# Kernel optimization log

Hardware: AMD Instinct MI355X
Metric: run time of the kernel (lower is better)

## Reference

```python
import jax, jax.numpy as jnp
import numpy as np

B, C, T, H = 256, 8, 512, 512  # batch, channels(6 arms + 2 time), timesteps, hidden
OUT = 2


def setup_inputs() -> dict:
    key = jax.random.key(0)
    ks = jax.random.split(key, 8)
    # arm lengths positive and away from 0 (denominator 0.15*arm in likelihood)
    arms = jax.random.uniform(ks[0], (B, 6, T), minval=0.5, maxval=1.5)
    tm = jax.random.uniform(ks[1], (B, 2, T))
    inputs = jnp.concatenate([arms, tm], axis=1)  # (B, 8, T)
    s_in = 1.0 / np.sqrt(6.0)
    s_rec = 1.0 / np.sqrt(float(H))
    W_in = jax.random.uniform(ks[2], (H, 6), minval=-s_in, maxval=s_in)
    b_in = jax.random.uniform(ks[3], (H,), minval=-s_in, maxval=s_in)
    W_rec = jax.random.uniform(ks[4], (H, H), minval=-s_rec, maxval=s_rec)
    b_rec = jax.random.uniform(ks[5], (H,), minval=-s_rec, maxval=s_rec)
    W_key = jax.random.uniform(ks[6], (OUT, H), minval=-s_rec, maxval=s_rec)
    b_key = jax.random.uniform(ks[7], (OUT,), minval=-s_rec, maxval=s_rec)
    return {"inputs": inputs, "W_in": W_in, "b_in": b_in,
            "W_rec": W_rec, "b_rec": b_rec, "W_key": W_key, "b_key": b_key}


def _likelihood(tm, arms):
    # tm: (B,), arms: (B, n) -> squared normalized timing mismatch; zero rows where tm==0
    prs = jnp.square((tm[:, None] - arms) / (0.15 * arms))
    return jnp.where(tm[:, None] == 0, 0.0, prs)


def reference(inputs, W_in, b_in, W_rec, b_rec, W_key, b_key):
    Bn, Cn, Tn = inputs.shape
    Hn = W_rec.shape[0]
    xs = jnp.transpose(inputs, (2, 0, 1))[1:]  # (T-1, B, 8); loop starts at t=1
    key0 = jnp.ones((Bn,), dtype=inputs.dtype)
    h0 = jnp.zeros((Bn, Hn), dtype=inputs.dtype)

    def step(carry, x_t):
        key_h_pre, h_pre = carry
        arms_pri = x_t[:, :2]
        arms_sec = x_t[:, 2:6]
        tm = x_t[:, 6:8]
        # gate secondary arms by previous key
        arms_sum = arms_sec[:, :2] * key_h_pre[:, None] + arms_sec[:, 2:] * (1.0 - key_h_pre)[:, None]
        prs_t = jnp.concatenate([_likelihood(tm[:, 0], arms_pri),
                                 _likelihood(tm[:, 1], arms_sum)], axis=1)  # (B, 4)
        inp_t = jnp.concatenate([arms_pri, arms_sum, tm], axis=1)  # (B, 6)
        h_t = jnp.tanh(inp_t @ W_in.T + b_in + h_pre @ W_rec.T + b_rec)  # (B, H)
        key_t = jax.nn.sigmoid(h_t @ W_key.T + b_key)  # (B, 2)
        return (key_t[:, 0], h_t), (key_t, prs_t, h_t)

    _, (keys, prs, hs) = jax.lax.scan(step, (key0, h0), xs)
    # prepend the t=0 zero slice and move time to last axis, matching torch buffers
    keys = jnp.concatenate([jnp.zeros((1, Bn, OUT), keys.dtype), keys], axis=0).transpose(1, 2, 0)
    prs = jnp.concatenate([jnp.zeros((1, Bn, 2 * OUT), prs.dtype), prs], axis=0).transpose(1, 2, 0)
    hs = jnp.concatenate([jnp.zeros((1, Bn, Hn), hs.dtype), hs], axis=0).transpose(1, 2, 0)
    tm_modified = inputs[:, -2:, :]
    return keys, prs, hs, tm_modified
```

## Files before the change

kernel.cpp:

```cpp
#include <hip/hip_runtime.h>

#define TDS 512
#define NBATCH 256

typedef _Float16 h2 __attribute__((ext_vector_type(2)));

__device__ __forceinline__ unsigned int pack2(float lo, float hi) {
    h2 v;
    v.x = (_Float16)lo;
    v.y = (_Float16)hi;
    return __builtin_bit_cast(unsigned int, v);
}
__device__ __forceinline__ h2 uph(unsigned int u) {
    return __builtin_bit_cast(h2, u);
}

#if __has_builtin(__builtin_amdgcn_fdot2)
__device__ __forceinline__ float fdot2(h2 w, h2 x, float acc) {
    return __builtin_amdgcn_fdot2(w, x, acc, false);
}
#else
__device__ __forceinline__ float fdot2(h2 w, h2 x, float acc) {
    return fmaf((float)w.x, (float)x.x, fmaf((float)w.y, (float)x.y, acc));
}
#endif

__device__ __forceinline__ float fast_rcp(float x) {
#if __has_builtin(__builtin_amdgcn_rcpf)
    return __builtin_amdgcn_rcpf(x);
#else
    return 1.0f / x;
#endif
}

__device__ __forceinline__ float fast_tanh(float x) {
    return 1.0f - 2.0f * fast_rcp(1.0f + __expf(2.0f * x));
}
__device__ __forceinline__ float fast_sigmoid(float x) {
    return fast_rcp(1.0f + __expf(-x));
}

#define KEYS_OFF 0u
#define PRS_OFF  262144u
#define HS_OFF   786432u
#define TM_OFF   67895296u

#define HP_CHUNK 72
#define HP_BUF   (4 * HP_CHUNK)

__device__ __forceinline__ void flush_window(
    float* __restrict__ g_out, int b, int tid, int w,
    const float* __restrict__ lds_hst,
    const float (*__restrict__ lds_kst)[2],
    const float (*__restrict__ lds_pst)[4])
{
    const int tbase = w * 8;
    float h[8];
#pragma unroll
    for (int s = 0; s < 8; ++s) h[s] = lds_hst[s * TDS + tid];
    float4* dst = (float4*)(g_out + HS_OFF + (unsigned)b * 262144u + (unsigned)tid * 512u + (unsigned)tbase);
    dst[0] = make_float4(h[0], h[1], h[2], h[3]);
    dst[1] = make_float4(h[4], h[5], h[6], h[7]);

    if (tid < 2) {
        float k[8];
#pragma unroll
        for (int s = 0; s < 8; ++s) k[s] = lds_kst[s][tid];
        float4* kd = (float4*)(g_out + KEYS_OFF + (unsigned)b * 1024u + (unsigned)tid * 512u + (unsigned)tbase);
        kd[0] = make_float4(k[0], k[1], k[2], k[3]);
        kd[1] = make_float4(k[4], k[5], k[6], k[7]);
    } else if (tid < 6) {
        const int o = tid - 2;
        float p[8];
#pragma unroll
        for (int s = 0; s < 8; ++s) p[s] = lds_pst[s][o];
        float4* pd = (float4*)(g_out + PRS_OFF + (unsigned)b * 2048u + (unsigned)o * 512u + (unsigned)tbase);
        pd[0] = make_float4(p[0], p[1], p[2], p[3]);
        pd[1] = make_float4(p[4], p[5], p[6], p[7]);
    }
}

__global__ __launch_bounds__(TDS, 1) void rnn_att_kernel(
    const float* __restrict__ g_inputs,
    const float* __restrict__ g_Win,
    const float* __restrict__ g_bin,
    const float* __restrict__ g_Wrec,
    const float* __restrict__ g_brec,
    const float* __restrict__ g_Wkey,
    const float* __restrict__ g_bkey,
    float* __restrict__ g_out)
{
    __shared__ __attribute__((aligned(16))) unsigned int lds_w[64][TDS];
    __shared__ __attribute__((aligned(16))) unsigned int lds_hp[2 * HP_BUF];
    __shared__ __attribute__((aligned(16))) float lds_hst[8 * TDS];
    __shared__ __attribute__((aligned(16))) float lds_ksum[2][16];
    __shared__ float lds_kst[8][2];
    __shared__ float lds_pst[8][4];

    const int tid = threadIdx.x;
    const int b = blockIdx.x;
    const int kc = tid & 3;
    const int rg = tid >> 2;
    const int r_out = tid;

    unsigned int wreg[192];
#pragma unroll
    for (int i = 0; i < 4; ++i) {
        const int r = (rg << 2) + i;
        const float4* src = (const float4*)(g_Wrec + r * 512 + kc * 128);
#pragma unroll
        for (int g = 0; g < 16; ++g) {
            float4 f0 = src[2 * g];
            float4 f1 = src[2 * g + 1];
            unsigned int u0 = pack2(f0.x, f0.y);
            unsigned int u1 = pack2(f0.z, f0.w);
            unsigned int u2 = pack2(f1.x, f1.y);
            unsigned int u3 = pack2(f1.z, f1.w);
            if (g < 12) {
                wreg[i * 48 + g * 4 + 0] = u0;
                wreg[i * 48 + g * 4 + 1] = u1;
                wreg[i * 48 + g * 4 + 2] = u2;
                wreg[i * 48 + g * 4 + 3] = u3;
            } else {
                const int pbase = i * 16 + (g - 12) * 4;
                lds_w[pbase + 0][tid] = u0;
                lds_w[pbase + 1][tid] = u1;
                lds_w[pbase + 2][tid] = u2;
                lds_w[pbase + 3][tid] = u3;
            }
        }
    }

    float win[6];
#pragma unroll
    for (int j = 0; j < 6; ++j) win[j] = g_Win[r_out * 6 + j];
    const float bias = g_bin[r_out] + g_brec[r_out];
    const float wk0 = g_Wkey[r_out];
    const float wk1 = g_Wkey[512 + r_out];
    const float bk0 = g_bkey[0];
    const float bk1 = g_bkey[1];

    lds_hp[tid] = 0u;
    if (tid < 2 * HP_BUF - TDS) lds_hp[TDS + tid] = 0u;

    if (tid < 256) {
        const float4* s = (const float4*)(g_inputs + b * 4096 + 3072);
        float4* d = (float4*)(g_out + TM_OFF + (unsigned)b * 1024u);
        d[tid] = s[tid];
    }
    __syncthreads();

    const float* gin = g_inputs + b * 4096;
    float key_pre = 1.0f;
    float xv[8];

    for (int t = 0; t < 512; ++t) {
        const int s = t & 7;
        if (s == 0 && t > 0) {
            __syncthreads();
            flush_window(g_out, b, tid, (t >> 3) - 1, lds_hst, lds_kst, lds_pst);
            __syncthreads();
        }

        float xn[8];
        {
            const int tn = (t < 511) ? t + 1 : 511;
#pragma unroll
            for (int j = 0; j < 8; ++j) xn[j] = gin[512 * j + tn];
        }

        float h_new = 0.0f, p0 = 0.0f, p1 = 0.0f, p2 = 0.0f, p3 = 0.0f;
        if (t > 0) {
            float x0 = xv[0], x1 = xv[1], x2 = xv[2], x3 = xv[3];
            float x4 = xv[4], x5 = xv[5], x6 = xv[6], x7 = xv[7];
            float as0 = x2 * key_pre + x4 * (1.0f - key_pre);
            float as1 = x3 * key_pre + x5 * (1.0f - key_pre);
            float wd = bias;
            wd = fmaf(x0, win[0], wd);
            wd = fmaf(x1, win[1], wd);
            wd = fmaf(as0, win[2], wd);
            wd = fmaf(as1, win[3], wd);
            wd = fmaf(x6, win[4], wd);
            wd = fmaf(x7, win[5], wd);
            {
                float q0 = (x6 - x0) / (0.15f * x0);
                float q1 = (x6 - x1) / (0.15f * x1);
                float q2 = (x7 - as0) / (0.15f * as0);
                float q3 = (x7 - as1) / (0.15f * as1);
                p0 = q0 * q0; p1 = q1 * q1; p2 = q2 * q2; p3 = q3 * q3;
                if (x6 == 0.0f) { p0 = 0.0f; p1 = 0.0f; }
                if (x7 == 0.0f) { p2 = 0.0f; p3 = 0.0f; }
            }
            const unsigned int* hb = lds_hp + ((t - 1) & 1) * HP_BUF + kc * HP_CHUNK;
            float a[4] = {0.0f, 0.0f, 0.0f, 0.0f};
#pragma unroll
            for (int c = 0; c < 12; ++c) {
                uint4 hu = ((const uint4*)hb)[c];
                h2 x0h = uph(hu.x), x1h = uph(hu.y), x2h = uph(hu.z), x3h = uph(hu.w);
#pragma unroll
                for (int i = 0; i < 4; ++i) {
                    a[i] = fdot2(uph(wreg[i * 48 + 4 * c + 0]), x0h, a[i]);
                    a[i] = fdot2(uph(wreg[i * 48 + 4 * c + 1]), x1h, a[i]);
                    a[i] = fdot2(uph(wreg[i * 48 + 4 * c + 2]), x2h, a[i]);
                    a[i] = fdot2(uph(wreg[i * 48 + 4 * c + 3]), x3h, a[i]);
                }
            }
#pragma unroll
            for (int c = 0; c < 4; ++c) {
                uint4 hu = ((const uint4*)(hb + 48))[c];
                h2 x0h = uph(hu.x), x1h = uph(hu.y), x2h = uph(hu.z), x3h = uph(hu.w);
#pragma unroll
                for (int i = 0; i < 4; ++i) {
                    a[i] = fdot2(uph(lds_w[i * 16 + 4 * c + 0][tid]), x0h, a[i]);
                    a[i] = fdot2(uph(lds_w[i * 16 + 4 * c + 1][tid]), x1h, a[i]);
                    a[i] = fdot2(uph(lds_w[i * 16 + 4 * c + 2][tid]), x2h, a[i]);
                    a[i] = fdot2(uph(lds_w[i * 16 + 4 * c + 3][tid]), x3h, a[i]);
                }
            }
#pragma unroll
            for (int i = 0; i < 4; ++i) {
                a[i] += __shfl_xor(a[i], 1, 64);
                a[i] += __shfl_xor(a[i], 2, 64);
            }
            float rsum = a[0];
            if (kc == 1) rsum = a[1];
            if (kc == 2) rsum = a[2];
            if (kc == 3) rsum = a[3];
            h_new = fast_tanh(rsum + wd);

            float h_other = __shfl_xor(h_new, 1, 64);
            if ((tid & 1) == 0) {
                const int p = tid >> 1;
                lds_hp[(t & 1) * HP_BUF + (p >> 6) * HP_CHUNK + (p & 63)] = pack2(h_new, h_other);
            }

            float kp0 = h_new * wk0, kp1 = h_new * wk1;
#pragma unroll
            for (int m = 1; m < 64; m <<= 1) {
                kp0 += __shfl_xor(kp0, m, 64);
                kp1 += __shfl_xor(kp1, m, 64);
            }
            if ((tid & 63) == 0) {
                lds_ksum[t & 1][(tid >> 6) * 2 + 0] = kp0;
                lds_ksum[t & 1][(tid >> 6) * 2 + 1] = kp1;
            }
            if (tid == 0) {
                lds_pst[s][0] = p0; lds_pst[s][1] = p1;
                lds_pst[s][2] = p2; lds_pst[s][3] = p3;
            }
        } else {
            if (tid == 0) {
                lds_pst[s][0] = 0.0f; lds_pst[s][1] = 0.0f;
                lds_pst[s][2] = 0.0f; lds_pst[s][3] = 0.0f;
            }
        }
        lds_hst[s * TDS + r_out] = h_new;

        __syncthreads();

        float k0 = 0.0f, k1 = 0.0f;
        if (t > 0) {
            const float4* ks = (const float4*)&lds_ksum[t & 1][0];
            float4 v0 = ks[0], v1 = ks[1], v2 = ks[2], v3 = ks[3];
            float s0 = ((v0.x + v1.x) + (v2.x + v3.x)) + ((v0.z + v1.z) + (v2.z + v3.z));
            float s1 = ((v0.y + v1.y) + (v2.y + v3.y)) + ((v0.w + v1.w) + (v2.w + v3.w));
            k0 = fast_sigmoid(s0 + bk0);
            k1 = fast_sigmoid(s1 + bk1);
            key_pre = k0;
        }
        if (tid == 0) { lds_kst[s][0] = k0; lds_kst[s][1] = k1; }

#pragma unroll
        for (int j = 0; j < 8; ++j) xv[j] = xn[j];
    }

    __syncthreads();
    flush_window(g_out, b, tid, 63, lds_hst, lds_kst, lds_pst);
}

extern "C" void kernel_launch(void* const* d_in, const int* in_sizes, int n_in,
                              void* d_out, int out_size, void* d_ws, size_t ws_size,
                              hipStream_t stream) {
    rnn_att_kernel<<<dim3(NBATCH), dim3(TDS), 0, stream>>>(
        (const float*)d_in[0],
        (const float*)d_in[1],
        (const float*)d_in[2],
        (const float*)d_in[3],
        (const float*)d_in[4],
        (const float*)d_in[5],
        (const float*)d_in[6],
        (float*)d_out);
}
```

Before: 1.898 ms.

## Restructure RNN time loop to one barrier per step with double-buffered staging

Rotates the loop so the key reduction from the previous step is read right after the single per-step barrier. The separate flush barriers are removed by double-buffering the key and likelihood staging arrays and passing the current key in registers. The key-dependent input projection is refactored into a single fma, and the likelihood divisions move to thread 0 using fast reciprocals. This cuts the barriers per step from one plus two every eight steps down to one, at the cost of slightly lower likelihood precision and more intricate slot and parity indexing.

Measured after the change: 2.016 ms. 1.06x slower.

```diff
diff --git a/kernel.cpp b/kernel.cpp
--- a/kernel.cpp
+++ b/kernel.cpp
@@ -51,8 +51,9 @@
 __device__ __forceinline__ void flush_window(
     float* __restrict__ g_out, int b, int tid, int w,
     const float* __restrict__ lds_hst,
-    const float (*__restrict__ lds_kst)[2],
-    const float (*__restrict__ lds_pst)[4])
+    const float (*__restrict__ kst)[2],
+    const float (*__restrict__ pst)[4],
+    float k0loc, float k1loc)
 {
     const int tbase = w * 8;
     float h[8];
@@ -65,7 +66,8 @@
     if (tid < 2) {
         float k[8];
 #pragma unroll
-        for (int s = 0; s < 8; ++s) k[s] = lds_kst[s][tid];
+        for (int s = 0; s < 7; ++s) k[s] = kst[s][tid];
+        k[7] = (tid == 0) ? k0loc : k1loc;
         float4* kd = (float4*)(g_out + KEYS_OFF + (unsigned)b * 1024u + (unsigned)tid * 512u + (unsigned)tbase);
         kd[0] = make_float4(k[0], k[1], k[2], k[3]);
         kd[1] = make_float4(k[4], k[5], k[6], k[7]);
@@ -73,7 +75,7 @@
         const int o = tid - 2;
         float p[8];
 #pragma unroll
-        for (int s = 0; s < 8; ++s) p[s] = lds_pst[s][o];
+        for (int s = 0; s < 8; ++s) p[s] = pst[s][o];
         float4* pd = (float4*)(g_out + PRS_OFF + (unsigned)b * 2048u + (unsigned)o * 512u + (unsigned)tbase);
         pd[0] = make_float4(p[0], p[1], p[2], p[3]);
         pd[1] = make_float4(p[4], p[5], p[6], p[7]);
@@ -94,8 +96,8 @@
     __shared__ __attribute__((aligned(16))) unsigned int lds_hp[2 * HP_BUF];
     __shared__ __attribute__((aligned(16))) float lds_hst[8 * TDS];
     __shared__ __attribute__((aligned(16))) float lds_ksum[2][16];
-    __shared__ float lds_kst[8][2];
-    __shared__ float lds_pst[8][4];
+    __shared__ float lds_kst[2][8][2];
+    __shared__ float lds_pst[2][8][4];
 
     const int tid = threadIdx.x;
     const int b = blockIdx.x;
@@ -148,134 +150,152 @@
         float4* d = (float4*)(g_out + TM_OFF + (unsigned)b * 1024u);
         d[tid] = s[tid];
     }
+
+    lds_hst[tid] = 0.0f;
+    if (tid == 0) {
+        lds_pst[0][0][0] = 0.0f; lds_pst[0][0][1] = 0.0f;
+        lds_pst[0][0][2] = 0.0f; lds_pst[0][0][3] = 0.0f;
+        lds_kst[0][0][0] = 0.0f; lds_kst[0][0][1] = 0.0f;
+    }
     __syncthreads();
 
     const float* gin = g_inputs + b * 4096;
     float key_pre = 1.0f;
     float xv[8];
-
-    for (int t = 0; t < 512; ++t) {
-        const int s = t & 7;
-        if (s == 0 && t > 0) {
-            __syncthreads();
-            flush_window(g_out, b, tid, (t >> 3) - 1, lds_hst, lds_kst, lds_pst);
-            __syncthreads();
-        }
-
-        float xn[8];
-        {
-            const int tn = (t < 511) ? t + 1 : 511;
-#pragma unroll
-            for (int j = 0; j < 8; ++j) xn[j] = gin[512 * j + tn];
-        }
-
-        float h_new = 0.0f, p0 = 0.0f, p1 = 0.0f, p2 = 0.0f, p3 = 0.0f;
-        if (t > 0) {
-            float x0 = xv[0], x1 = xv[1], x2 = xv[2], x3 = xv[3];
-            float x4 = xv[4], x5 = xv[5], x6 = xv[6], x7 = xv[7];
-            float as0 = x2 * key_pre + x4 * (1.0f - key_pre);
-            float as1 = x3 * key_pre + x5 * (1.0f - key_pre);
-            float wd = bias;
-            wd = fmaf(x0, win[0], wd);
-            wd = fmaf(x1, win[1], wd);
-            wd = fmaf(as0, win[2], wd);
-            wd = fmaf(as1, win[3], wd);
-            wd = fmaf(x6, win[4], wd);
-            wd = fmaf(x7, win[5], wd);
-            {
-                float q0 = (x6 - x0) / (0.15f * x0);
-                float q1 = (x6 - x1) / (0.15f * x1);
-                float q2 = (x7 - as0) / (0.15f * as0);
-                float q3 = (x7 - as1) / (0.15f * as1);
-                p0 = q0 * q0; p1 = q1 * q1; p2 = q2 * q2; p3 = q3 * q3;
-                if (x6 == 0.0f) { p0 = 0.0f; p1 = 0.0f; }
-                if (x7 == 0.0f) { p2 = 0.0f; p3 = 0.0f; }
-            }
-            const unsigned int* hb = lds_hp + ((t - 1) & 1) * HP_BUF + kc * HP_CHUNK;
-            float a[4] = {0.0f, 0.0f, 0.0f, 0.0f};
-#pragma unroll
-            for (int c = 0; c < 12; ++c) {
-                uint4 hu = ((const uint4*)hb)[c];
-                h2 x0h = uph(hu.x), x1h = uph(hu.y), x2h = uph(hu.z), x3h = uph(hu.w);
-#pragma unroll
-                for (int i = 0; i < 4; ++i) {
-                    a[i] = fdot2(uph(wreg[i * 48 + 4 * c + 0]), x0h, a[i]);
-                    a[i] = fdot2(uph(wreg[i * 48 + 4 * c + 1]), x1h, a[i]);
-                    a[i] = fdot2(uph(wreg[i * 48 + 4 * c + 2]), x2h, a[i]);
-                    a[i] = fdot2(uph(wreg[i * 48 + 4 * c + 3]), x3h, a[i]);
-                }
-            }
-#pragma unroll
-            for (int c = 0; c < 4; ++c) {
-                uint4 hu = ((const uint4*)(hb + 48))[c];
-                h2 x0h = uph(hu.x), x1h = uph(hu.y), x2h = uph(hu.z), x3h = uph(hu.w);
-#pragma unroll
-                for (int i = 0; i < 4; ++i) {
-                    a[i] = fdot2(uph(lds_w[i * 16 + 4 * c + 0][tid]), x0h, a[i]);
-                    a[i] = fdot2(uph(lds_w[i * 16 + 4 * c + 1][tid]), x1h, a[i]);
-                    a[i] = fdot2(uph(lds_w[i * 16 + 4 * c + 2][tid]), x2h, a[i]);
-                    a[i] = fdot2(uph(lds_w[i * 16 + 4 * c + 3][tid]), x3h, a[i]);
-                }
-            }
-#pragma unroll
-            for (int i = 0; i < 4; ++i) {
-                a[i] += __shfl_xor(a[i], 1, 64);
-                a[i] += __shfl_xor(a[i], 2, 64);
-            }
-            float rsum = a[0];
-            if (kc == 1) rsum = a[1];
-            if (kc == 2) rsum = a[2];
-            if (kc == 3) rsum = a[3];
-            h_new = fast_tanh(rsum + wd);
-
-            float h_other = __shfl_xor(h_new, 1, 64);
-            if ((tid & 1) == 0) {
-                const int p = tid >> 1;
-                lds_hp[(t & 1) * HP_BUF + (p >> 6) * HP_CHUNK + (p & 63)] = pack2(h_new, h_other);
-            }
-
-            float kp0 = h_new * wk0, kp1 = h_new * wk1;
-#pragma unroll
-            for (int m = 1; m < 64; m <<= 1) {
-                kp0 += __shfl_xor(kp0, m, 64);
-                kp1 += __shfl_xor(kp1, m, 64);
-            }
-            if ((tid & 63) == 0) {
-                lds_ksum[t & 1][(tid >> 6) * 2 + 0] = kp0;
-                lds_ksum[t & 1][(tid >> 6) * 2 + 1] = kp1;
-            }
-            if (tid == 0) {
-                lds_pst[s][0] = p0; lds_pst[s][1] = p1;
-                lds_pst[s][2] = p2; lds_pst[s][3] = p3;
-            }
-        } else {
-            if (tid == 0) {
-                lds_pst[s][0] = 0.0f; lds_pst[s][1] = 0.0f;
-                lds_pst[s][2] = 0.0f; lds_pst[s][3] = 0.0f;
-            }
-        }
-        lds_hst[s * TDS + r_out] = h_new;
-
+#pragma unroll
+    for (int j = 0; j < 8; ++j) xv[j] = gin[512 * j + 1];
+
+    for (int t = 1; t < 512; ++t) {
         __syncthreads();
 
         float k0 = 0.0f, k1 = 0.0f;
-        if (t > 0) {
-            const float4* ks = (const float4*)&lds_ksum[t & 1][0];
+        if (t > 1) {
+            const float4* ks = (const float4*)&lds_ksum[(t - 1) & 1][0];
             float4 v0 = ks[0], v1 = ks[1], v2 = ks[2], v3 = ks[3];
             float s0 = ((v0.x + v1.x) + (v2.x + v3.x)) + ((v0.z + v1.z) + (v2.z + v3.z));
             float s1 = ((v0.y + v1.y) + (v2.y + v3.y)) + ((v0.w + v1.w) + (v2.w + v3.w));
             k0 = fast_sigmoid(s0 + bk0);
             k1 = fast_sigmoid(s1 + bk1);
             key_pre = k0;
-        }
-        if (tid == 0) { lds_kst[s][0] = k0; lds_kst[s][1] = k1; }
+            if (tid == 0) {
+                const int slot = (t - 1) & 7;
+                const int par = ((t - 1) >> 3) & 1;
+                lds_kst[par][slot][0] = k0;
+                lds_kst[par][slot][1] = k1;
+            }
+        }
+
+        if ((t & 7) == 0) {
+            const int w = (t >> 3) - 1;
+            flush_window(g_out, b, tid, w, lds_hst, lds_kst[w & 1], lds_pst[w & 1], k0, k1);
+        }
+
+        float xn[8];
+        {
+            const int tn = (t < 511) ? t + 1 : 511;
+#pragma unroll
+            for (int j = 0; j < 8; ++j) xn[j] = gin[512 * j + tn];
+        }
+
+        const float x0 = xv[0], x1 = xv[1], x2 = xv[2], x3 = xv[3];
+        const float x4 = xv[4], x5 = xv[5], x6 = xv[6], x7 = xv[7];
+        float wd = bias;
+        wd = fmaf(x0, win[0], wd);
+        wd = fmaf(x1, win[1], wd);
+        wd = fmaf(x4, win[2], wd);
+        wd = fmaf(x5, win[3], wd);
+        wd = fmaf(x6, win[4], wd);
+        wd = fmaf(x7, win[5], wd);
+        const float wdk = (x2 - x4) * win[2] + (x3 - x5) * win[3];
+        wd = fmaf(key_pre, wdk, wd);
+
+        const unsigned int* hb = lds_hp + ((t - 1) & 1) * HP_BUF + kc * HP_CHUNK;
+        float a[4] = {0.0f, 0.0f, 0.0f, 0.0f};
+#pragma unroll
+        for (int c = 0; c < 12; ++c) {
+            uint4 hu = ((const uint4*)hb)[c];
+            h2 x0h = uph(hu.x), x1h = uph(hu.y), x2h = uph(hu.z), x3h = uph(hu.w);
+#pragma unroll
+            for (int i = 0; i < 4; ++i) {
+                a[i] = fdot2(uph(wreg[i * 48 + 4 * c + 0]), x0h, a[i]);
+                a[i] = fdot2(uph(wreg[i * 48 + 4 * c + 1]), x1h, a[i]);
+                a[i] = fdot2(uph(wreg[i * 48 + 4 * c + 2]), x2h, a[i]);
+                a[i] = fdot2(uph(wreg[i * 48 + 4 * c + 3]), x3h, a[i]);
+            }
+        }
+#pragma unroll
+        for (int c = 0; c < 4; ++c) {
+            uint4 hu = ((const uint4*)(hb + 48))[c];
+            h2 x0h = uph(hu.x), x1h = uph(hu.y), x2h = uph(hu.z), x3h = uph(hu.w);
+#pragma unroll
+            for (int i = 0; i < 4; ++i) {
+                a[i] = fdot2(uph(lds_w[i * 16 + 4 * c + 0][tid]), x0h, a[i]);
+                a[i] = fdot2(uph(lds_w[i * 16 + 4 * c + 1][tid]), x1h, a[i]);
+                a[i] = fdot2(uph(lds_w[i * 16 + 4 * c + 2][tid]), x2h, a[i]);
+                a[i] = fdot2(uph(lds_w[i * 16 + 4 * c + 3][tid]), x3h, a[i]);
+            }
+        }
+#pragma unroll
+        for (int i = 0; i < 4; ++i) {
+            a[i] += __shfl_xor(a[i], 1, 64);
+            a[i] += __shfl_xor(a[i], 2, 64);
+        }
+        float rsum = a[0];
+        if (kc == 1) rsum = a[1];
+        if (kc == 2) rsum = a[2];
+        if (kc == 3) rsum = a[3];
+        const float h_new = fast_tanh(rsum + wd);
+
+        const float h_other = __shfl_xor(h_new, 1, 64);
+        if ((tid & 1) == 0) {
+            const int p = tid >> 1;
+            lds_hp[(t & 1) * HP_BUF + (p >> 6) * HP_CHUNK + (p & 63)] = pack2(h_new, h_other);
+        }
+        lds_hst[(t & 7) * TDS + r_out] = h_new;
+
+        float kp0 = h_new * wk0, kp1 = h_new * wk1;
+#pragma unroll
+        for (int m = 1; m < 64; m <<= 1) {
+            kp0 += __shfl_xor(kp0, m, 64);
+            kp1 += __shfl_xor(kp1, m, 64);
+        }
+        if ((tid & 63) == 0) {
+            lds_ksum[t & 1][(tid >> 6) * 2 + 0] = kp0;
+            lds_ksum[t & 1][(tid >> 6) * 2 + 1] = kp1;
+        }
+
+        if (tid == 0) {
+            const float as0 = fmaf(key_pre, x2 - x4, x4);
+            const float as1 = fmaf(key_pre, x3 - x5, x5);
+            const float q0 = (x6 - x0) * fast_rcp(0.15f * x0);
+            const float q1 = (x6 - x1) * fast_rcp(0.15f * x1);
+            const float q2 = (x7 - as0) * fast_rcp(0.15f * as0);
+            const float q3 = (x7 - as1) * fast_rcp(0.15f * as1);
+            float p0 = q0 * q0, p1 = q1 * q1, p2 = q2 * q2, p3 = q3 * q3;
+            if (x6 == 0.0f) { p0 = 0.0f; p1 = 0.0f; }
+            if (x7 == 0.0f) { p2 = 0.0f; p3 = 0.0f; }
+            const int par = (t >> 3) & 1;
+            lds_pst[par][t & 7][0] = p0;
+            lds_pst[par][t & 7][1] = p1;
+            lds_pst[par][t & 7][2] = p2;
+            lds_pst[par][t & 7][3] = p3;
+        }
 
 #pragma unroll
         for (int j = 0; j < 8; ++j) xv[j] = xn[j];
     }
 
     __syncthreads();
-    flush_window(g_out, b, tid, 63, lds_hst, lds_kst, lds_pst);
+    float k0, k1;
+    {
+        const float4* ks = (const float4*)&lds_ksum[1][0];
+        float4 v0 = ks[0], v1 = ks[1], v2 = ks[2], v3 = ks[3];
+        float s0 = ((v0.x + v1.x) + (v2.x + v3.x)) + ((v0.z + v1.z) + (v2.z + v3.z));
+        float s1 = ((v0.y + v1.y) + (v2.y + v3.y)) + ((v0.w + v1.w) + (v2.w + v3.w));
+        k0 = fast_sigmoid(s0 + bk0);
+        k1 = fast_sigmoid(s1 + bk1);
+    }
+    flush_window(g_out, b, tid, 63, lds_hst, lds_kst[1], lds_pst[1], k0, k1);
 }
 
 extern "C" void kernel_launch(void* const* d_in, const int* in_sizes, int n_in,
```
